# Optimization experiments

Measured on AMD Instinct MI355X. Metric: run time of the kernel, lower is better.

The kernel has to match this reference:

```python
import jax, jax.numpy as jnp
import numpy as np

GRID_MIN, GRID_MAX, NUM_GRIDS = -1.2, 0.2, 8
INV_DENOMINATOR = 0.5


def setup_inputs() -> dict:
    key = jax.random.key(0)
    x = jax.random.normal(key, (16, 64, 128, 128), dtype=jnp.float32)
    grid = jnp.linspace(GRID_MIN, GRID_MAX, NUM_GRIDS, dtype=jnp.float32)
    inv_denominator = jnp.asarray(INV_DENOMINATOR, dtype=jnp.float32)
    return {"x": x, "grid": grid, "inv_denominator": inv_denominator}


def reference(x, grid, inv_denominator):
    # RSWAF basis: res = 1 - tanh((x - g) * inv_denominator)^2  (sech^2 bump)
    # broadcast x [B,C,H,W] against grid [G] -> [B,C,H,W,G]
    th = jnp.tanh((x[..., None] - grid) * inv_denominator)
    return 1.0 - th * th
```

## Files before the change

### kernel.cpp

```cpp
#include <hip/hip_runtime.h>


typedef float v4f __attribute__((ext_vector_type(4)));

__global__ __launch_bounds__(256) void rswaf_kernel(
    const float* __restrict__ x,
    const float* __restrict__ grid,
    const float* __restrict__ inv_den_p,
    v4f* __restrict__ out,
    int n4)
{
    const float c = fabsf(inv_den_p[0]) * 2.8853900817779268f;

    const v4f g0 = ((const v4f*)grid)[0];
    const v4f g1 = ((const v4f*)grid)[1];

    const int stride = gridDim.x * blockDim.x;
    for (int j = blockIdx.x * blockDim.x + threadIdx.x; j < n4; j += stride) {
        const float xi = __builtin_nontemporal_load(&x[j >> 1]);
        const v4f g = (j & 1) ? g1 : g0;

        float d0 = fabsf(xi - g.x);
        float d1 = fabsf(xi - g.y);
        float d2 = fabsf(xi - g.z);
        float d3 = fabsf(xi - g.w);
        float u0 = __builtin_amdgcn_exp2f(-c * d0);
        float u1 = __builtin_amdgcn_exp2f(-c * d1);
        float u2 = __builtin_amdgcn_exp2f(-c * d2);
        float u3 = __builtin_amdgcn_exp2f(-c * d3);
        float t0 = 1.0f + u0, t1 = 1.0f + u1, t2 = 1.0f + u2, t3 = 1.0f + u3;
        v4f r;
        r.x = 4.0f * u0 * __builtin_amdgcn_rcpf(t0 * t0);
        r.y = 4.0f * u1 * __builtin_amdgcn_rcpf(t1 * t1);
        r.z = 4.0f * u2 * __builtin_amdgcn_rcpf(t2 * t2);
        r.w = 4.0f * u3 * __builtin_amdgcn_rcpf(t3 * t3);

        __builtin_nontemporal_store(r, &out[j]);
    }
}

extern "C" void kernel_launch(void* const* d_in, const int* in_sizes, int n_in,
                              void* d_out, int out_size, void* d_ws, size_t ws_size,
                              hipStream_t stream) {
    const float* x       = (const float*)d_in[0];
    const float* grid    = (const float*)d_in[1];
    const float* inv_den = (const float*)d_in[2];
    float* out = (float*)d_out;

    const int n4 = out_size / 4;
    const int block = 256;
    int nblocks = (n4 + block - 1) / block;
    if (nblocks > 2048) nblocks = 2048;
    rswaf_kernel<<<nblocks, block, 0, stream>>>(x, grid, inv_den,
                                                (v4f*)out, n4);
}
```

Before: 581.0 us.

## Share one exp2 across the four grid points and unroll the loop by four

Each thread always touches the same half of the grid, because the stride is even. The kernel therefore precomputes exp2(C*(g_k-g_0)) once per thread and gets u_k = u0*p_k, so it needs one transcendental per input instead of four. The abs-based form is replaced by a signed exponent clamped to ±100, which relies on the sech² identity being symmetric. The grid-stride loop is also unrolled by four, issuing four independent loads up front to raise memory-level parallelism. The risk is overflow or precision loss when a large u0 is multiplied by p_k for inputs far from the grid.

```diff
diff --git a/kernel.cpp b/kernel.cpp
--- a/kernel.cpp
+++ b/kernel.cpp
@@ -10,32 +10,47 @@
     v4f* __restrict__ out,
     int n4)
 {
-    const float c = fabsf(inv_den_p[0]) * 2.8853900817779268f;
+    const float C = fabsf(inv_den_p[0]) * 2.8853900817779268f;
 
-    const v4f g0 = ((const v4f*)grid)[0];
-    const v4f g1 = ((const v4f*)grid)[1];
+    int j = blockIdx.x * blockDim.x + threadIdx.x;
+    const int stride = gridDim.x * blockDim.x;
 
-    const int stride = gridDim.x * blockDim.x;
-    for (int j = blockIdx.x * blockDim.x + threadIdx.x; j < n4; j += stride) {
-        const float xi = __builtin_nontemporal_load(&x[j >> 1]);
-        const v4f g = (j & 1) ? g1 : g0;
+    const v4f g = ((const v4f*)grid)[j & 1];
 
-        float d0 = fabsf(xi - g.x);
-        float d1 = fabsf(xi - g.y);
-        float d2 = fabsf(xi - g.z);
-        float d3 = fabsf(xi - g.w);
-        float u0 = __builtin_amdgcn_exp2f(-c * d0);
-        float u1 = __builtin_amdgcn_exp2f(-c * d1);
-        float u2 = __builtin_amdgcn_exp2f(-c * d2);
-        float u3 = __builtin_amdgcn_exp2f(-c * d3);
+    const float cgx = C * g.x;
+    const float p1 = __builtin_amdgcn_exp2f(C * (g.y - g.x));
+    const float p2 = __builtin_amdgcn_exp2f(C * (g.z - g.x));
+    const float p3 = __builtin_amdgcn_exp2f(C * (g.w - g.x));
+    const float q1 = 4.0f * p1, q2 = 4.0f * p2, q3 = 4.0f * p3;
+
+    auto body = [&](float xi, int idx) {
+        float e0 = fmaf(-C, xi, cgx);
+        e0 = fminf(fmaxf(e0, -100.0f), 100.0f);
+        float u0 = __builtin_amdgcn_exp2f(e0);
+        float u1 = u0 * p1, u2 = u0 * p2, u3 = u0 * p3;
         float t0 = 1.0f + u0, t1 = 1.0f + u1, t2 = 1.0f + u2, t3 = 1.0f + u3;
         v4f r;
-        r.x = 4.0f * u0 * __builtin_amdgcn_rcpf(t0 * t0);
-        r.y = 4.0f * u1 * __builtin_amdgcn_rcpf(t1 * t1);
-        r.z = 4.0f * u2 * __builtin_amdgcn_rcpf(t2 * t2);
-        r.w = 4.0f * u3 * __builtin_amdgcn_rcpf(t3 * t3);
+        r.x = (4.0f * u0) * __builtin_amdgcn_rcpf(t0 * t0);
+        r.y = (u0 * q1)   * __builtin_amdgcn_rcpf(t1 * t1);
+        r.z = (u0 * q2)   * __builtin_amdgcn_rcpf(t2 * t2);
+        r.w = (u0 * q3)   * __builtin_amdgcn_rcpf(t3 * t3);
+        __builtin_nontemporal_store(r, &out[idx]);
+    };
 
-        __builtin_nontemporal_store(r, &out[j]);
+    const int nfull = n4 - 3 * stride;
+    for (; j < nfull; j += 4 * stride) {
+        const int ja = j, jb = j + stride, jc = j + 2 * stride, jd = j + 3 * stride;
+        float xa = __builtin_nontemporal_load(&x[ja >> 1]);
+        float xb = __builtin_nontemporal_load(&x[jb >> 1]);
+        float xc = __builtin_nontemporal_load(&x[jc >> 1]);
+        float xd = __builtin_nontemporal_load(&x[jd >> 1]);
+        body(xa, ja);
+        body(xb, jb);
+        body(xc, jc);
+        body(xd, jd);
+    }
+    for (; j < n4; j += stride) {
+        body(__builtin_nontemporal_load(&x[j >> 1]), j);
     }
 }
 
```

New measurement: 578.1 us. Within noise of the previous version (-0.5%).
